# Kernel tuning notes

Measured on AMD Instinct MI355X. Metric: run time of the kernel, lower is better.

Reference implementation:

```python
import jax, jax.numpy as jnp
import numpy as np

N_NODES = 50000
N_EDGES = 800000
IN_DIM, HID_DIM, OUT_DIM = 128, 128, 64


def setup_inputs() -> dict:
    key = jax.random.key(0)
    ks = jax.random.split(key, 12)
    x = jax.random.normal(ks[0], (N_NODES, IN_DIM), dtype=jnp.float32)
    src = jax.random.randint(ks[1], (N_EDGES,), 0, N_NODES, dtype=jnp.int32)
    dst = jax.random.randint(ks[2], (N_EDGES,), 0, N_NODES, dtype=jnp.int32)
    def lin(k, fan_in, fan_out):
        s = 1.0 / np.sqrt(fan_in)
        kw, kb = jax.random.split(k)
        W = jax.random.uniform(kw, (fan_in, fan_out), jnp.float32, -s, s)
        b = jax.random.uniform(kb, (fan_out,), jnp.float32, -s, s)
        return W, b
    W1, b1 = lin(ks[3], IN_DIM, HID_DIM)
    W2, b2 = lin(ks[4], HID_DIM, HID_DIM)
    W3, b3 = lin(ks[5], HID_DIM, OUT_DIM)
    Wf, bf = lin(ks[6], OUT_DIM, 1)
    return {"x": x, "src": src, "dst": dst,
            "W1": W1, "b1": b1, "W2": W2, "b2": b2,
            "W3": W3, "b3": b3, "Wf": Wf, "bf": bf}


def reference(x, src, dst, W1, b1, W2, b2, W3, b3, Wf, bf):
    n = x.shape[0]
    # GCN symmetric norm with self-loops: deg = in-degree + 1 (self loop)
    ones = jnp.ones(src.shape[0], x.dtype)
    deg = jax.ops.segment_sum(ones, dst, num_segments=n) + 1.0
    dinv = jax.lax.rsqrt(deg)                       # [N]
    edge_norm = dinv[src] * dinv[dst]               # [E]
    self_norm = dinv * dinv                         # [N], self-loop weight

    def gcn(h, W, b):
        h = h @ W                                   # transform first (PyG order)
        agg = jax.ops.segment_sum(h[src] * edge_norm[:, None], dst, num_segments=n)
        agg = agg + h * self_norm[:, None]          # self-loop contribution
        return agg + b

    h = jax.nn.relu(gcn(x, W1, b1))
    h = jax.nn.relu(gcn(h, W2, b2))
    h = jax.nn.relu(gcn(h, W3, b3))
    return h @ Wf + bf                              # [N, 1] per-node scores
```

## Files before the change

### kernel.cpp

```cpp
#include <hip/hip_runtime.h>
#include <hip/hip_bf16.h>

typedef short bf16x8 __attribute__((ext_vector_type(8)));
typedef float f32x4 __attribute__((ext_vector_type(4)));
typedef _Float16 f16x2 __attribute__((ext_vector_type(2)));
typedef unsigned int u32;

static __device__ __forceinline__ unsigned short f2bf_rne(float f) {
    unsigned int u = __float_as_uint(f);
    u += 0x7fff + ((u >> 16) & 1);
    return (unsigned short)(u >> 16);
}
static __device__ __forceinline__ float bf2f(unsigned short h) {
    return __uint_as_float(((unsigned int)h) << 16);
}
static __device__ __forceinline__ u32 packsplit(float f) {
    unsigned short h = f2bf_rne(f);
    unsigned short l = f2bf_rne(f - bf2f(h));
    return ((u32)h << 16) | l;
}

static __device__ __forceinline__ void wsplit_one(const float* W, unsigned short* hi,
                                                  unsigned short* lo, int BN, int idx) {
    int k = idx / BN, n = idx % BN;
    float w = W[idx];
    unsigned short h = f2bf_rne(w);
    unsigned short l = f2bf_rne(w - bf2f(h));
    int CT = BN >> 4;
    int kc = k >> 5, quad = (k >> 3) & 3, j = k & 7;
    int ct = n >> 4, c = n & 15;
    int slot = (((kc * CT + ct) * 4 + quad) * 16 + c) * 8 + j;
    hi[slot] = h;
    lo[slot] = l;
}


template<int BN>
static __device__ __forceinline__ void gemm_body(const u32* __restrict__ A,
                        const unsigned short* __restrict__ Whi, const unsigned short* __restrict__ Wlo,
                        _Float16* __restrict__ C, int N, int blk) {
    constexpr int CT = BN / 16;
    const int tid = threadIdx.x;
    const int wave = tid >> 6;
    const int lane = tid & 63;
    const int quad = lane >> 4;
    const int c16 = lane & 15;
    const int row0 = blk * 64;

    const int arow = row0 + wave * 16 + c16;
    const bool valid = arow < N;
    const u32* ar = A + (size_t)arow * 128;

    uint4 a[8];
    #pragma unroll
    for (int i = 0; i < 8; ++i) {
        int off = (i >> 1) * 32 + quad * 8 + (i & 1) * 4;
        a[i] = valid ? *(const uint4*)&ar[off] : make_uint4(0, 0, 0, 0);
    }

    f32x4 acc[CT];
    #pragma unroll
    for (int t = 0; t < CT; ++t) acc[t] = (f32x4){0.f, 0.f, 0.f, 0.f};

    #pragma unroll
    for (int kc = 0; kc < 4; ++kc) {
        uint4 a0 = a[kc * 2], a1 = a[kc * 2 + 1];
        union { u32 u[4]; bf16x8 v; } hi, lo;
        hi.u[0] = (a0.x >> 16) | (a0.y & 0xffff0000u);
        hi.u[1] = (a0.z >> 16) | (a0.w & 0xffff0000u);
        hi.u[2] = (a1.x >> 16) | (a1.y & 0xffff0000u);
        hi.u[3] = (a1.z >> 16) | (a1.w & 0xffff0000u);
        lo.u[0] = (a0.x & 0xffffu) | (a0.y << 16);
        lo.u[1] = (a0.z & 0xffffu) | (a0.w << 16);
        lo.u[2] = (a1.x & 0xffffu) | (a1.y << 16);
        lo.u[3] = (a1.z & 0xffffu) | (a1.w << 16);

        #pragma unroll
        for (int ct = 0; ct < CT; ++ct) {
            size_t bslot = ((size_t)(kc * CT + ct) * 64 + lane) * 8;
            bf16x8 bhi = *(const bf16x8*)&Whi[bslot];
            bf16x8 blo = *(const bf16x8*)&Wlo[bslot];
            acc[ct] = __builtin_amdgcn_mfma_f32_16x16x32_bf16(hi.v, bhi, acc[ct], 0, 0, 0);
            acc[ct] = __builtin_amdgcn_mfma_f32_16x16x32_bf16(hi.v, blo, acc[ct], 0, 0, 0);
            acc[ct] = __builtin_amdgcn_mfma_f32_16x16x32_bf16(lo.v, bhi, acc[ct], 0, 0, 0);
        }
    }

    #pragma unroll
    for (int ct = 0; ct < CT; ++ct) {
        #pragma unroll
        for (int r = 0; r < 4; ++r) {
            int grow = row0 + wave * 16 + quad * 4 + r;
            if (grow < N) C[(size_t)grow * BN + ct * 16 + c16] = (_Float16)acc[ct][r];
        }
    }
}


__global__ __launch_bounds__(256) void k_count_wsplit(const int* __restrict__ dst, int* __restrict__ deg,
                          int* __restrict__ rank,
                          const float* __restrict__ W1, const float* __restrict__ W2, const float* __restrict__ W3,
                          unsigned short* __restrict__ W1hi, unsigned short* __restrict__ W1lo,
                          unsigned short* __restrict__ W2hi, unsigned short* __restrict__ W2lo,
                          unsigned short* __restrict__ W3hi, unsigned short* __restrict__ W3lo,
                          int E) {
    int e = blockIdx.x * blockDim.x + threadIdx.x;
    if (e < E) rank[e] = atomicAdd(&deg[dst[e]], 1);
    if (e < 128 * 128) {
        wsplit_one(W1, W1hi, W1lo, 128, e);
        wsplit_one(W2, W2hi, W2lo, 128, e);
    }
    if (e < 128 * 64) wsplit_one(W3, W3hi, W3lo, 64, e);
}

__global__ __launch_bounds__(1024) void k_scan_xsplit(const int* __restrict__ deg, float* __restrict__ dinv,
                                               int* __restrict__ row_start, int N, int NB,
                                               const float* __restrict__ x, u32* __restrict__ xsplit,
                                               int nF4) {
    const int t = threadIdx.x;
    if ((int)blockIdx.x >= NB) {
        int i = (blockIdx.x - NB) * 1024 + t;
        if (i < nF4) {
            float4 v = ((const float4*)x)[i];
            uint4 p;
            p.x = packsplit(v.x);
            p.y = packsplit(v.y);
            p.z = packsplit(v.z);
            p.w = packsplit(v.w);
            ((uint4*)xsplit)[i] = p;
        }
        return;
    }
    __shared__ int s[1024];
    __shared__ int wsum[16];
    __shared__ int prefix;
    const int base = blockIdx.x * 1024;

    {
        int v = 0;
        for (int j = t; j < base; j += 1024) v += deg[j];
        for (int off = 32; off > 0; off >>= 1) v += __shfl_down(v, off, 64);
        if ((t & 63) == 0) wsum[t >> 6] = v;
        __syncthreads();
        if (t == 0) {
            int acc = 0;
            #pragma unroll
            for (int k = 0; k < 16; ++k) acc += wsum[k];
            prefix = acc;
        }
    }

    int i = base + t;
    int v = 0;
    if (i < N) {
        v = deg[i];
        dinv[i] = rsqrtf((float)v + 1.0f);
    }
    s[t] = v;
    __syncthreads();
    for (int off = 1; off < 1024; off <<= 1) {
        int x2 = (t >= off) ? s[t - off] : 0;
        __syncthreads();
        s[t] += x2;
        __syncthreads();
    }
    if (i <= N) row_start[i] = prefix + s[t] - v;
}


__global__ __launch_bounds__(256, 3) void k_gemm1_scatter(const u32* __restrict__ A,
                          const unsigned short* __restrict__ Whi, const unsigned short* __restrict__ Wlo,
                          _Float16* __restrict__ C, int N, int gemmGrid,
                          const int* __restrict__ src, const int* __restrict__ dst,
                          const int* __restrict__ row_start, const int* __restrict__ rank,
                          const float* __restrict__ dinv, int2* __restrict__ cv, int E) {
    if ((int)blockIdx.x < gemmGrid) {
        gemm_body<128>(A, Whi, Wlo, C, N, blockIdx.x);
    } else {
        int e = (blockIdx.x - gemmGrid) * 256 + threadIdx.x;
        if (e < E) {
            int d = dst[e];
            int s = src[e];
            cv[row_start[d] + rank[e]] = make_int2(s, __float_as_int(dinv[s]));
        }
    }
}

template<int BN>
__global__ __launch_bounds__(256, 3) void k_gemm_mfma(const u32* __restrict__ A,
                        const unsigned short* __restrict__ Whi, const unsigned short* __restrict__ Wlo,
                        _Float16* __restrict__ C, int N) {
    gemm_body<BN>(A, Whi, Wlo, C, N, blockIdx.x);
}


__global__ __launch_bounds__(256) void k_agg128(const _Float16* __restrict__ t, u32* __restrict__ outp,
                      const int* __restrict__ row_start, const int2* __restrict__ cv,
                      const float* __restrict__ dinv, const float* __restrict__ bias,
                      int N) {
    int gid = blockIdx.x * blockDim.x + threadIdx.x;
    int node = gid >> 6;
    int lane = gid & 63;
    if (node >= N) return;
    int p = row_start[node];
    int end = row_start[node + 1];
    const f16x2* tp = (const f16x2*)t;
    float2 acc[4];
    #pragma unroll
    for (int j = 0; j < 4; ++j) acc[j] = make_float2(0.f, 0.f);

    while (p < end) {
        int idx = p + lane;
        int2 h = (idx < end) ? cv[idx] : make_int2(0, 0);
        int cnt = min(end - p, 64);
        int rounds = (cnt + 15) >> 4;
        for (int r = 0; r < rounds; ++r) {
            int base = r * 16;
            int s[16]; float w[16];
            #pragma unroll
            for (int j = 0; j < 16; ++j) {
                s[j] = __builtin_amdgcn_readlane(h.x, base + j);
                w[j] = __int_as_float(__builtin_amdgcn_readlane(h.y, base + j));
            }
            f16x2 v[16];
            #pragma unroll
            for (int j = 0; j < 16; ++j) v[j] = tp[s[j] * 64 + lane];
            #pragma unroll
            for (int j = 0; j < 16; ++j) {
                acc[j & 3].x += w[j] * (float)v[j].x;
                acc[j & 3].y += w[j] * (float)v[j].y;
            }
        }
        p += 64;
    }
    float di = dinv[node];
    f16x2 sv = tp[node * 64 + lane];
    float2 bv = ((const float2*)bias)[lane];
    float sx = (acc[0].x + acc[1].x) + (acc[2].x + acc[3].x);
    float sy = (acc[0].y + acc[1].y) + (acc[2].y + acc[3].y);
    float rx = fmaxf(di * sx + di * di * (float)sv.x + bv.x, 0.f);
    float ry = fmaxf(di * sy + di * di * (float)sv.y + bv.y, 0.f);
    ((uint2*)outp)[node * 64 + lane] = make_uint2(packsplit(rx), packsplit(ry));
}

__global__ __launch_bounds__(256) void k_agg64_final(const _Float16* __restrict__ t, float* __restrict__ outp,
                      const int* __restrict__ row_start, const int2* __restrict__ cv,
                      const float* __restrict__ dinv, const float* __restrict__ bias,
                      const float* __restrict__ Wf, const float* __restrict__ bf,
                      int N) {
    int gid = blockIdx.x * blockDim.x + threadIdx.x;
    int node = gid >> 6;
    int lane = gid & 63;
    if (node >= N) return;
    int p = row_start[node];
    int end = row_start[node + 1];
    float acc[4] = {0.f, 0.f, 0.f, 0.f};

    while (p < end) {
        int idx = p + lane;
        int2 h = (idx < end) ? cv[idx] : make_int2(0, 0);
        int cnt = min(end - p, 64);
        int rounds = (cnt + 15) >> 4;
        for (int r = 0; r < rounds; ++r) {
            int base = r * 16;
            int s[16]; float w[16];
            #pragma unroll
            for (int j = 0; j < 16; ++j) {
                s[j] = __builtin_amdgcn_readlane(h.x, base + j);
                w[j] = __int_as_float(__builtin_amdgcn_readlane(h.y, base + j));
            }
            _Float16 v[16];
            #pragma unroll
            for (int j = 0; j < 16; ++j) v[j] = t[s[j] * 64 + lane];
            #pragma unroll
            for (int j = 0; j < 16; ++j) acc[j & 3] += w[j] * (float)v[j];
        }
        p += 64;
    }
    float di = dinv[node];
    float r = di * ((acc[0] + acc[1]) + (acc[2] + acc[3])) + di * di * (float)t[node * 64 + lane] + bias[lane];
    r = fmaxf(r, 0.f);
    float v = r * Wf[lane];
    for (int off = 32; off > 0; off >>= 1) v += __shfl_down(v, off, 64);
    if (lane == 0) outp[node] = v + bf[0];
}


extern "C" void kernel_launch(void* const* d_in, const int* in_sizes, int n_in,
                              void* d_out, int out_size, void* d_ws, size_t ws_size,
                              hipStream_t stream) {
    const float* x  = (const float*)d_in[0];
    const int*   src = (const int*)d_in[1];
    const int*   dst = (const int*)d_in[2];
    const float* W1 = (const float*)d_in[3];
    const float* b1 = (const float*)d_in[4];
    const float* W2 = (const float*)d_in[5];
    const float* b2 = (const float*)d_in[6];
    const float* W3 = (const float*)d_in[7];
    const float* b3 = (const float*)d_in[8];
    const float* Wf = (const float*)d_in[9];
    const float* bf = (const float*)d_in[10];
    float* out = (float*)d_out;

    const int N = 50000;
    const int E = 800000;

    char* ws = (char*)d_ws;
    size_t off = 0;
    auto alloc = [&](size_t bytes) -> void* {
        void* p = (void*)(ws + off);
        off += (bytes + 511) & ~((size_t)511);
        return p;
    };
    int*   deg       = (int*)alloc((size_t)N * 4);
    float* dinv      = (float*)alloc((size_t)N * 4);
    int*   row_start = (int*)alloc((size_t)(N + 1) * 4);
    int*   rank      = (int*)alloc((size_t)E * 4);
    int2*  cv        = (int2*)alloc((size_t)E * 8);
    u32*   xsplit    = (u32*)alloc((size_t)N * 128 * 4);
    _Float16* bufT   = (_Float16*)alloc((size_t)N * 128 * 2);
    u32*   bufH      = (u32*)alloc((size_t)N * 128 * 4);
    unsigned short* W1hi = (unsigned short*)alloc(128 * 128 * 2);
    unsigned short* W1lo = (unsigned short*)alloc(128 * 128 * 2);
    unsigned short* W2hi = (unsigned short*)alloc(128 * 128 * 2);
    unsigned short* W2lo = (unsigned short*)alloc(128 * 128 * 2);
    unsigned short* W3hi = (unsigned short*)alloc(128 * 64 * 2);
    unsigned short* W3lo = (unsigned short*)alloc(128 * 64 * 2);

    hipMemsetAsync(deg, 0, (size_t)N * 4, stream);

    k_count_wsplit<<<(E + 255) / 256, 256, 0, stream>>>(dst, deg, rank, W1, W2, W3,
                                                        W1hi, W1lo, W2hi, W2lo, W3hi, W3lo, E);
    int NB = (N + 1023) / 1024;
    int nF4 = (N * 128) / 4;
    int xBlocks = (nF4 + 1023) / 1024;
    k_scan_xsplit<<<NB + xBlocks, 1024, 0, stream>>>(deg, dinv, row_start, N, NB, x, xsplit, nF4);

    int gemmGrid = (N + 63) / 64;
    int scatGrid = (E + 255) / 256;
    int aggGrid = (N * 64 + 255) / 256;

    k_gemm1_scatter<<<gemmGrid + scatGrid, 256, 0, stream>>>(xsplit, W1hi, W1lo, bufT, N, gemmGrid,
                                                             src, dst, row_start, rank, dinv, cv, E);
    k_agg128<<<aggGrid, 256, 0, stream>>>(bufT, bufH, row_start, cv, dinv, b1, N);
    k_gemm_mfma<128><<<gemmGrid, 256, 0, stream>>>(bufH, W2hi, W2lo, bufT, N);
    k_agg128<<<aggGrid, 256, 0, stream>>>(bufT, bufH, row_start, cv, dinv, b2, N);
    k_gemm_mfma<64><<<gemmGrid, 256, 0, stream>>>(bufH, W3hi, W3lo, bufT, N);
    k_agg64_final<<<aggGrid, 256, 0, stream>>>(bufT, out, row_start, cv, dinv, b3, Wf, bf, N);
}
```

Measured before the change: 277.0 us.

## Split degree-count atomics across eight sub-histograms to cut contention

Degree counting now spreads atomics over eight copies of the histogram, selected by block index. The scan sums the eight copies per node and also writes per-copy base offsets, which the CSR scatter uses to place each edge. The aim is less atomic contention on hot counters. In exchange it adds an 8x larger memset, eight strided reads per node in the scan (and in the prefix loop), and an extra base8 array read in the scatter.

```diff
diff --git a/kernel.cpp b/kernel.cpp
--- a/kernel.cpp
+++ b/kernel.cpp
@@ -97,15 +97,18 @@
 }
 
 
-__global__ __launch_bounds__(256) void k_count_wsplit(const int* __restrict__ dst, int* __restrict__ deg,
-                          int* __restrict__ rank,
+__global__ __launch_bounds__(256) void k_count_wsplit(const int* __restrict__ dst,
+                          int* __restrict__ deg8, int* __restrict__ rank,
                           const float* __restrict__ W1, const float* __restrict__ W2, const float* __restrict__ W3,
                           unsigned short* __restrict__ W1hi, unsigned short* __restrict__ W1lo,
                           unsigned short* __restrict__ W2hi, unsigned short* __restrict__ W2lo,
                           unsigned short* __restrict__ W3hi, unsigned short* __restrict__ W3lo,
-                          int E) {
+                          int E, int N) {
     int e = blockIdx.x * blockDim.x + threadIdx.x;
-    if (e < E) rank[e] = atomicAdd(&deg[dst[e]], 1);
+    if (e < E) {
+        int c = blockIdx.x & 7;
+        rank[e] = atomicAdd(&deg8[(size_t)c * N + dst[e]], 1);
+    }
     if (e < 128 * 128) {
         wsplit_one(W1, W1hi, W1lo, 128, e);
         wsplit_one(W2, W2hi, W2lo, 128, e);
@@ -113,8 +116,10 @@
     if (e < 128 * 64) wsplit_one(W3, W3hi, W3lo, 64, e);
 }
 
-__global__ __launch_bounds__(1024) void k_scan_xsplit(const int* __restrict__ deg, float* __restrict__ dinv,
-                                               int* __restrict__ row_start, int N, int NB,
+__global__ __launch_bounds__(1024) void k_scan_xsplit(const int* __restrict__ deg8,
+                                               float* __restrict__ dinv,
+                                               int* __restrict__ row_start, int* __restrict__ base8,
+                                               int N, int NB,
                                                const float* __restrict__ x, u32* __restrict__ xsplit,
                                                int nF4) {
     const int t = threadIdx.x;
@@ -138,7 +143,12 @@
 
     {
         int v = 0;
-        for (int j = t; j < base; j += 1024) v += deg[j];
+        for (int j = t; j < base; j += 1024) {
+            int vv = 0;
+            #pragma unroll
+            for (int k = 0; k < 8; ++k) vv += deg8[(size_t)k * N + j];
+            v += vv;
+        }
         for (int off = 32; off > 0; off >>= 1) v += __shfl_down(v, off, 64);
         if ((t & 63) == 0) wsum[t >> 6] = v;
         __syncthreads();
@@ -151,12 +161,17 @@
     }
 
     int i = base + t;
-    int v = 0;
+    int d[8];
+    int tot = 0;
     if (i < N) {
-        v = deg[i];
-        dinv[i] = rsqrtf((float)v + 1.0f);
-    }
-    s[t] = v;
+        #pragma unroll
+        for (int k = 0; k < 8; ++k) { d[k] = deg8[(size_t)k * N + i]; tot += d[k]; }
+        dinv[i] = rsqrtf((float)tot + 1.0f);
+    } else {
+        #pragma unroll
+        for (int k = 0; k < 8; ++k) d[k] = 0;
+    }
+    s[t] = tot;
     __syncthreads();
     for (int off = 1; off < 1024; off <<= 1) {
         int x2 = (t >= off) ? s[t - off] : 0;
@@ -164,7 +179,16 @@
         s[t] += x2;
         __syncthreads();
     }
-    if (i <= N) row_start[i] = prefix + s[t] - v;
+    int rs = prefix + s[t] - tot;
+    if (i <= N) row_start[i] = rs;
+    if (i < N) {
+        int bb[8];
+        int b = rs;
+        #pragma unroll
+        for (int k = 0; k < 8; ++k) { bb[k] = b; b += d[k]; }
+        *(uint4*)&base8[(size_t)i * 8]     = make_uint4(bb[0], bb[1], bb[2], bb[3]);
+        *(uint4*)&base8[(size_t)i * 8 + 4] = make_uint4(bb[4], bb[5], bb[6], bb[7]);
+    }
 }
 
 
@@ -172,7 +196,7 @@
                           const unsigned short* __restrict__ Whi, const unsigned short* __restrict__ Wlo,
                           _Float16* __restrict__ C, int N, int gemmGrid,
                           const int* __restrict__ src, const int* __restrict__ dst,
-                          const int* __restrict__ row_start, const int* __restrict__ rank,
+                          const int* __restrict__ base8, const int* __restrict__ rank,
                           const float* __restrict__ dinv, int2* __restrict__ cv, int E) {
     if ((int)blockIdx.x < gemmGrid) {
         gemm_body<128>(A, Whi, Wlo, C, N, blockIdx.x);
@@ -181,7 +205,8 @@
         if (e < E) {
             int d = dst[e];
             int s = src[e];
-            cv[row_start[d] + rank[e]] = make_int2(s, __float_as_int(dinv[s]));
+            int c = (e >> 8) & 7;
+            cv[base8[(size_t)d * 8 + c] + rank[e]] = make_int2(s, __float_as_int(dinv[s]));
         }
     }
 }
@@ -312,9 +337,10 @@
         off += (bytes + 511) & ~((size_t)511);
         return p;
     };
-    int*   deg       = (int*)alloc((size_t)N * 4);
+    int*   deg8      = (int*)alloc((size_t)8 * N * 4);
     float* dinv      = (float*)alloc((size_t)N * 4);
     int*   row_start = (int*)alloc((size_t)(N + 1) * 4);
+    int*   base8     = (int*)alloc((size_t)8 * N * 4);
     int*   rank      = (int*)alloc((size_t)E * 4);
     int2*  cv        = (int2*)alloc((size_t)E * 8);
     u32*   xsplit    = (u32*)alloc((size_t)N * 128 * 4);
@@ -327,21 +353,22 @@
     unsigned short* W3hi = (unsigned short*)alloc(128 * 64 * 2);
     unsigned short* W3lo = (unsigned short*)alloc(128 * 64 * 2);
 
-    hipMemsetAsync(deg, 0, (size_t)N * 4, stream);
-
-    k_count_wsplit<<<(E + 255) / 256, 256, 0, stream>>>(dst, deg, rank, W1, W2, W3,
-                                                        W1hi, W1lo, W2hi, W2lo, W3hi, W3lo, E);
+    hipMemsetAsync(deg8, 0, (size_t)8 * N * 4, stream);
+
+    k_count_wsplit<<<(E + 255) / 256, 256, 0, stream>>>(dst, deg8, rank, W1, W2, W3,
+                                                        W1hi, W1lo, W2hi, W2lo, W3hi, W3lo, E, N);
     int NB = (N + 1023) / 1024;
     int nF4 = (N * 128) / 4;
     int xBlocks = (nF4 + 1023) / 1024;
-    k_scan_xsplit<<<NB + xBlocks, 1024, 0, stream>>>(deg, dinv, row_start, N, NB, x, xsplit, nF4);
+    k_scan_xsplit<<<NB + xBlocks, 1024, 0, stream>>>(deg8, dinv, row_start, base8, N, NB,
+                                                     x, xsplit, nF4);
 
     int gemmGrid = (N + 63) / 64;
     int scatGrid = (E + 255) / 256;
     int aggGrid = (N * 64 + 255) / 256;
 
     k_gemm1_scatter<<<gemmGrid + scatGrid, 256, 0, stream>>>(xsplit, W1hi, W1lo, bufT, N, gemmGrid,
-                                                             src, dst, row_start, rank, dinv, cv, E);
+                                                             src, dst, base8, rank, dinv, cv, E);
     k_agg128<<<aggGrid, 256, 0, stream>>>(bufT, bufH, row_start, cv, dinv, b1, N);
     k_gemm_mfma<128><<<gemmGrid, 256, 0, stream>>>(bufH, W2hi, W2lo, bufT, N);
     k_agg128<<<aggGrid, 256, 0, stream>>>(bufT, bufH, row_start, cv, dinv, b2, N);
```

After: 286.0 us. 1.03x slower.
